# Performance work log

Measured on AMD Instinct MI355X. Metric: run time of the kernel, lower is better.

## Reference

```python
import jax, jax.numpy as jnp
import numpy as np
import math

NUM_HEADS = 16


def setup_inputs() -> dict:
    key = jax.random.key(0)
    ks = jax.random.split(key, 7)
    B, S, D = 2, 2048, 1024
    scale = 1.0 / math.sqrt(D)
    return {
        "query": jax.random.normal(ks[0], (B, S, D), jnp.float32),
        "key": jax.random.normal(ks[1], (B, S, D), jnp.float32),
        "value": jax.random.normal(ks[2], (B, S, D), jnp.float32),
        "Wq": jax.random.normal(ks[3], (D, D), jnp.float32) * scale,
        "Wk": jax.random.normal(ks[4], (D, D), jnp.float32) * scale,
        "Wv": jax.random.normal(ks[5], (D, D), jnp.float32) * scale,
        "Wo": jax.random.normal(ks[6], (D, D), jnp.float32) * scale,
    }


def reference(query, key, value, Wq, Wk, Wv, Wo):
    B, Sq, D = query.shape
    Sk = key.shape[1]
    H = NUM_HEADS
    dk = D // H
    # torch Linear (no bias): y = x @ W.T
    q = (query @ Wq.T).reshape(B, Sq, H, dk).transpose(0, 2, 1, 3)  # [B,H,Sq,dk]
    k = (key @ Wk.T).reshape(B, Sk, H, dk).transpose(0, 2, 1, 3)
    v = (value @ Wv.T).reshape(B, Sk, H, dk).transpose(0, 2, 1, 3)
    scores = jnp.einsum("bhqd,bhkd->bhqk", q, k) / jnp.sqrt(jnp.float32(dk))
    causal = jnp.tril(jnp.ones((Sq, Sk), dtype=bool))  # mask_future=True
    scores = jnp.where(causal[None, None], scores, jnp.float32(-1e9))
    p = jax.nn.softmax(scores, axis=-1)
    x = jnp.einsum("bhqk,bhkd->bhqd", p, v)  # [B,H,Sq,dk]
    x = x.transpose(0, 2, 1, 3).reshape(B, Sq, D)
    return x @ Wo.T
```

## Files before the change

### kernel.cpp

```cpp
#include <hip/hip_runtime.h>
#include <hip/hip_bf16.h>
#include <stdint.h>

#define D_MODEL 1024
#define NHEADS  16
#define DK      64
#define SEQ     2048
#define BATCH   2

typedef __bf16 bf16x8 __attribute__((ext_vector_type(8)));
typedef __bf16 bf16x4 __attribute__((ext_vector_type(4)));
typedef float  f32x4  __attribute__((ext_vector_type(4)));

__device__ __forceinline__ void async_copy16(const void* g, void* l) {
  __builtin_amdgcn_global_load_lds(
      (__attribute__((address_space(1))) void*)g,
      (__attribute__((address_space(3))) void*)l, 16, 0, 0);
}

__global__ void cast3(const float* __restrict__ a, const float* __restrict__ b,
                      const float* __restrict__ c, __bf16* __restrict__ oa,
                      __bf16* __restrict__ ob, __bf16* __restrict__ oc, int n) {
  const float* in = blockIdx.z == 0 ? a : blockIdx.z == 1 ? b : c;
  __bf16* out     = blockIdx.z == 0 ? oa : blockIdx.z == 1 ? ob : oc;
  int i = (blockIdx.x * blockDim.x + threadIdx.x) * 4;
  if (i < n) {
    float4 v = *(const float4*)(in + i);
    bf16x4 o;
    o.x = (__bf16)v.x; o.y = (__bf16)v.y; o.z = (__bf16)v.z; o.w = (__bf16)v.w;
    *(bf16x4*)(out + i) = o;
  }
}

__global__ void cast4(const float* __restrict__ a, const float* __restrict__ b,
                      const float* __restrict__ c, const float* __restrict__ d,
                      __bf16* __restrict__ oa, __bf16* __restrict__ ob,
                      __bf16* __restrict__ oc, __bf16* __restrict__ od, int n) {
  const float* in = blockIdx.z == 0 ? a : blockIdx.z == 1 ? b : blockIdx.z == 2 ? c : d;
  __bf16* out     = blockIdx.z == 0 ? oa : blockIdx.z == 1 ? ob : blockIdx.z == 2 ? oc : od;
  int i = (blockIdx.x * blockDim.x + threadIdx.x) * 4;
  if (i < n) {
    float4 v = *(const float4*)(in + i);
    bf16x4 o;
    o.x = (__bf16)v.x; o.y = (__bf16)v.y; o.z = (__bf16)v.z; o.w = (__bf16)v.w;
    *(bf16x4*)(out + i) = o;
  }
}

template <int BM, int BN, typename OutT>
__global__ __launch_bounds__(256, 2)
void gemm_bt(const __bf16* __restrict__ A0, const __bf16* __restrict__ A1, const __bf16* __restrict__ A2,
             const __bf16* __restrict__ B0, const __bf16* __restrict__ B1, const __bf16* __restrict__ B2,
             OutT* __restrict__ C0, OutT* __restrict__ C1, OutT* __restrict__ C2,
             int M, int N, int K) {
  constexpr int MI = BM / 32, NJ = BN / 32;
  const __bf16* A; const __bf16* Bm; OutT* C;
  if (blockIdx.z == 0)      { A = A0; Bm = B0; C = C0; }
  else if (blockIdx.z == 1) { A = A1; Bm = B1; C = C1; }
  else                      { A = A2; Bm = B2; C = C2; }

  __shared__ __bf16 Ash[BM * 32];
  __shared__ __bf16 Bsh[BN * 32];

  const int tid  = threadIdx.x;
  const int lane = tid & 63;
  const int w    = tid >> 6;
  const int quad = lane >> 4;
  const int l16  = lane & 15;
  const int wr   = w >> 1, wc = w & 1;
  const size_t m0 = (size_t)blockIdx.y * BM;
  const size_t n0 = (size_t)blockIdx.x * BN;

  f32x4 acc[MI][NJ] = {};

  for (int k0 = 0; k0 < K; k0 += 32) {
#pragma unroll
    for (int it = 0; it < BM / 64; ++it) {
      int slot = tid + it * 256;
      async_copy16(A + (m0 + (slot >> 2)) * K + k0 + (slot & 3) * 8, &Ash[slot * 8]);
    }
#pragma unroll
    for (int it = 0; it < BN / 64; ++it) {
      int slot = tid + it * 256;
      async_copy16(Bm + (n0 + (slot >> 2)) * K + k0 + (slot & 3) * 8, &Bsh[slot * 8]);
    }
    __syncthreads();
    bf16x8 af[MI], bfr[NJ];
#pragma unroll
    for (int i = 0; i < MI; ++i)
      af[i] = *(const bf16x8*)&Ash[(wr * (BM / 2) + i * 16 + l16) * 32 + quad * 8];
#pragma unroll
    for (int j = 0; j < NJ; ++j)
      bfr[j] = *(const bf16x8*)&Bsh[(wc * (BN / 2) + j * 16 + l16) * 32 + quad * 8];
#pragma unroll
    for (int i = 0; i < MI; ++i)
#pragma unroll
      for (int j = 0; j < NJ; ++j)
        acc[i][j] = __builtin_amdgcn_mfma_f32_16x16x32_bf16(af[i], bfr[j], acc[i][j], 0, 0, 0);
    __syncthreads();
  }

#pragma unroll
  for (int i = 0; i < MI; ++i)
#pragma unroll
    for (int j = 0; j < NJ; ++j)
#pragma unroll
      for (int r = 0; r < 4; ++r) {
        size_t row = m0 + wr * (BM / 2) + i * 16 + quad * 4 + r;
        size_t col = n0 + wc * (BN / 2) + j * 16 + l16;
        C[row * N + col] = (OutT)acc[i][j][r];
      }
}

__global__ __launch_bounds__(256, 4)
void transpose_v(const __bf16* __restrict__ Vp, __bf16* __restrict__ Vt) {
  __shared__ __bf16 L[64 * 64];
  const int t  = threadIdx.x;
  const int s0 = blockIdx.x * 64, d0 = blockIdx.y * 64, b = blockIdx.z;
#pragma unroll
  for (int it = 0; it < 2; ++it) {
    int slot = t + it * 256;
    int sl = slot >> 3, c = slot & 7;
    int4 v = *(const int4*)&Vp[((size_t)(b * SEQ + s0 + sl)) * D_MODEL + d0 + c * 8];
    *(int4*)&L[sl * 64 + ((c ^ (sl >> 3)) << 3)] = v;
  }
  __syncthreads();
#pragma unroll
  for (int it = 0; it < 2; ++it) {
    int slot = t + it * 256;
    int dl = slot >> 3, c2 = slot & 7;
    __bf16 tmp[8];
#pragma unroll
    for (int e = 0; e < 8; ++e) {
      int rr = c2 * 8 + e;
      tmp[e] = L[rr * 64 + (((dl >> 3) ^ c2) << 3) + (dl & 7)];
    }
    *(int4*)&Vt[((size_t)(b * D_MODEL + d0 + dl)) * SEQ + s0 + c2 * 8] = *(int4*)tmp;
  }
}

#define PS_STRIDE 72

__global__ __launch_bounds__(256, 2)
void attn_kernel(const __bf16* __restrict__ Qp, const __bf16* __restrict__ Kp,
                 const __bf16* __restrict__ Vt, __bf16* __restrict__ Xo) {
  __shared__ __bf16 Kbuf[2][2][64 * 32];
  __shared__ __bf16 Vbuf[2][2][64 * 32];
  __shared__ __bf16 Ps[64 * PS_STRIDE];

  const int tid  = threadIdx.x;
  const int lane = tid & 63;
  const int w    = tid >> 6;
  const int quad = lane >> 4;
  const int l16  = lane & 15;
  const int bh   = blockIdx.x;
  const int pair = blockIdx.y;
  const int b    = bh >> 4, h = bh & 15;
  const size_t baseRow = (size_t)b * SEQ;
  const int colBase = h * DK;

  const int srow = w * 16 + (lane >> 2);
  const int sk   = (lane & 3) * 8;

  const float c1 = 0.18033688011f;
  const float c2 = -23.083120654f;

#pragma unroll 1
  for (int half = 0; half < 2; ++half) {
    const int qt = half == 0 ? (31 - pair) : pair;
    const int q0 = qt * 64;

    bf16x8 aq0, aq1;
    {
      const __bf16* qrow = Qp + (baseRow + q0 + w * 16 + l16) * D_MODEL + colBase;
      aq0 = *(const bf16x8*)(qrow + quad * 8);
      aq1 = *(const bf16x8*)(qrow + 32 + quad * 8);
    }

    f32x4 oacc[4] = {};
    float plsum[4] = {0.f, 0.f, 0.f, 0.f};

    __syncthreads();
    {
      const __bf16* kbase = Kp + (baseRow + srow) * D_MODEL + colBase + sk;
      async_copy16(kbase,      &Kbuf[0][0][srow * 32 + sk]);
      async_copy16(kbase + 32, &Kbuf[0][1][srow * 32 + sk]);
      const __bf16* vbase = Vt + ((size_t)b * D_MODEL + colBase + srow) * SEQ + sk;
      async_copy16(vbase,      &Vbuf[0][0][srow * 32 + sk]);
      async_copy16(vbase + 32, &Vbuf[0][1][srow * 32 + sk]);
    }

    for (int j = 0; j <= qt; ++j) {
      const int bf = j & 1;
      __syncthreads();

      if (j < qt) {
        const int nb = bf ^ 1;
        const __bf16* kbase = Kp + (baseRow + (size_t)(j + 1) * 64 + srow) * D_MODEL + colBase + sk;
        async_copy16(kbase,      &Kbuf[nb][0][srow * 32 + sk]);
        async_copy16(kbase + 32, &Kbuf[nb][1][srow * 32 + sk]);
        const __bf16* vbase = Vt + ((size_t)b * D_MODEL + colBase + srow) * SEQ + (size_t)(j + 1) * 64 + sk;
        async_copy16(vbase,      &Vbuf[nb][0][srow * 32 + sk]);
        async_copy16(vbase + 32, &Vbuf[nb][1][srow * 32 + sk]);
      }

      f32x4 sacc[4] = {};
#pragma unroll
      for (int nt = 0; nt < 4; ++nt) {
        bf16x8 bk = *(const bf16x8*)&Kbuf[bf][0][(nt * 16 + l16) * 32 + quad * 8];
        sacc[nt] = __builtin_amdgcn_mfma_f32_16x16x32_bf16(aq0, bk, sacc[nt], 0, 0, 0);
      }
#pragma unroll
      for (int nt = 0; nt < 4; ++nt) {
        bf16x8 bk = *(const bf16x8*)&Kbuf[bf][1][(nt * 16 + l16) * 32 + quad * 8];
        sacc[nt] = __builtin_amdgcn_mfma_f32_16x16x32_bf16(aq1, bk, sacc[nt], 0, 0, 0);
      }

      const bool diag = (j == qt);
      const int rowg = q0 + w * 16 + quad * 4;
      const int colg = j * 64 + l16;
#pragma unroll
      for (int nt = 0; nt < 4; ++nt)
#pragma unroll
        for (int r = 0; r < 4; ++r) {
          float arg = fmaf(sacc[nt][r], c1, c2);
          if (diag && (colg + nt * 16 > rowg + r)) arg = -1e30f;
          float p = __builtin_amdgcn_exp2f(arg);
          plsum[r] += p;
          Ps[(w * 16 + quad * 4 + r) * PS_STRIDE + nt * 16 + l16] = (__bf16)p;
        }

#pragma unroll
      for (int kc = 0; kc < 2; ++kc) {
        bf16x8 ap = *(const bf16x8*)&Ps[(w * 16 + l16) * PS_STRIDE + kc * 32 + quad * 8];
#pragma unroll
        for (int no = 0; no < 4; ++no) {
          bf16x8 bv = *(const bf16x8*)&Vbuf[bf][kc][(no * 16 + l16) * 32 + quad * 8];
          oacc[no] = __builtin_amdgcn_mfma_f32_16x16x32_bf16(ap, bv, oacc[no], 0, 0, 0);
        }
      }
    }

#pragma unroll
    for (int r = 0; r < 4; ++r) {
      float l = plsum[r];
      for (int off = 1; off < 16; off <<= 1) l += __shfl_xor(l, off, 64);
      float inv = 1.0f / l;
#pragma unroll
      for (int no = 0; no < 4; ++no) {
        size_t row = baseRow + q0 + w * 16 + quad * 4 + r;
        Xo[row * D_MODEL + colBase + no * 16 + l16] = (__bf16)(oacc[no][r] * inv);
      }
    }
  }
}

extern "C" void kernel_launch(void* const* d_in, const int* in_sizes, int n_in,
                              void* d_out, int out_size, void* d_ws, size_t ws_size,
                              hipStream_t stream) {
  const float* q  = (const float*)d_in[0];
  const float* k  = (const float*)d_in[1];
  const float* v  = (const float*)d_in[2];
  const float* wq = (const float*)d_in[3];
  const float* wk = (const float*)d_in[4];
  const float* wv = (const float*)d_in[5];
  const float* wo = (const float*)d_in[6];
  float* out = (float*)d_out;

  const size_t MD = (size_t)BATCH * SEQ * D_MODEL;
  const size_t WD = (size_t)D_MODEL * D_MODEL;
  __bf16* ws  = (__bf16*)d_ws;
  __bf16* Qp  = ws;
  __bf16* Kp  = Qp + MD;
  __bf16* Vp  = Kp + MD;
  __bf16* Xa  = Vp + MD;
  __bf16* qbf = Xa + MD;
  __bf16* kbf = qbf + MD;
  __bf16* vbf = kbf + MD;
  __bf16* wqb = vbf + MD;
  __bf16* wkb = wqb + WD;
  __bf16* wvb = wkb + WD;
  __bf16* wob = wvb + WD;
  __bf16* Vt  = qbf;

  cast3<<<dim3((int)(MD / 1024), 1, 3), 256, 0, stream>>>(q, k, v, qbf, kbf, vbf, (int)MD);
  cast4<<<dim3((int)(WD / 1024), 1, 4), 256, 0, stream>>>(wq, wk, wv, wo, wqb, wkb, wvb, wob, (int)WD);

  gemm_bt<128, 128, __bf16><<<dim3(8, 32, 3), 256, 0, stream>>>(
      qbf, kbf, vbf, wqb, wkb, wvb, Qp, Kp, Vp,
      BATCH * SEQ, D_MODEL, D_MODEL);

  transpose_v<<<dim3(SEQ / 64, D_MODEL / 64, BATCH), 256, 0, stream>>>(Vp, Vt);

  attn_kernel<<<dim3(BATCH * NHEADS, 16), 256, 0, stream>>>(Qp, Kp, Vt, Xa);

  gemm_bt<64, 128, float><<<dim3(8, 64, 1), 256, 0, stream>>>(
      Xa, Xa, Xa, wob, wob, wob, out, out, out,
      BATCH * SEQ, D_MODEL, D_MODEL);
}
```

Measured before the change: 215.3 us.

## Split attention warps across key halves, merge casts, swap GEMM grid order

The attention kernel now gives each of the four warps a 32-row query slab and one half of each 64-key block. Partial outputs and row sums are combined through shared memory at the end, and occupancy is raised to 3 blocks per CU. The two cast kernels are merged into one launch. The GEMM grid mapping is swapped so consecutive blocks walk along M and reuse the same weight tile. The V transpose switches from an XOR swizzle to a padded shared-memory layout with scalar stores. The extra reduction step and the scalar LDS writes in the transpose add cost, and the higher occupancy target may squeeze registers.

Measured after the change: 323.8 us. +50.3%, slower.

```diff
diff --git a/kernel.cpp b/kernel.cpp
--- a/kernel.cpp
+++ b/kernel.cpp
@@ -18,33 +18,32 @@
       (__attribute__((address_space(3))) void*)l, 16, 0, 0);
 }
 
-__global__ void cast3(const float* __restrict__ a, const float* __restrict__ b,
-                      const float* __restrict__ c, __bf16* __restrict__ oa,
-                      __bf16* __restrict__ ob, __bf16* __restrict__ oc, int n) {
-  const float* in = blockIdx.z == 0 ? a : blockIdx.z == 1 ? b : c;
-  __bf16* out     = blockIdx.z == 0 ? oa : blockIdx.z == 1 ? ob : oc;
-  int i = (blockIdx.x * blockDim.x + threadIdx.x) * 4;
-  if (i < n) {
-    float4 v = *(const float4*)(in + i);
-    bf16x4 o;
-    o.x = (__bf16)v.x; o.y = (__bf16)v.y; o.z = (__bf16)v.z; o.w = (__bf16)v.w;
-    *(bf16x4*)(out + i) = o;
-  }
-}
-
-__global__ void cast4(const float* __restrict__ a, const float* __restrict__ b,
-                      const float* __restrict__ c, const float* __restrict__ d,
-                      __bf16* __restrict__ oa, __bf16* __restrict__ ob,
-                      __bf16* __restrict__ oc, __bf16* __restrict__ od, int n) {
-  const float* in = blockIdx.z == 0 ? a : blockIdx.z == 1 ? b : blockIdx.z == 2 ? c : d;
-  __bf16* out     = blockIdx.z == 0 ? oa : blockIdx.z == 1 ? ob : blockIdx.z == 2 ? oc : od;
-  int i = (blockIdx.x * blockDim.x + threadIdx.x) * 4;
-  if (i < n) {
-    float4 v = *(const float4*)(in + i);
-    bf16x4 o;
-    o.x = (__bf16)v.x; o.y = (__bf16)v.y; o.z = (__bf16)v.z; o.w = (__bf16)v.w;
-    *(bf16x4*)(out + i) = o;
-  }
+__global__ void cast_all(const float* __restrict__ q, const float* __restrict__ k,
+                         const float* __restrict__ v, const float* __restrict__ wq,
+                         const float* __restrict__ wk, const float* __restrict__ wv,
+                         const float* __restrict__ wo,
+                         __bf16* __restrict__ oq, __bf16* __restrict__ ok,
+                         __bf16* __restrict__ ov, __bf16* __restrict__ owq,
+                         __bf16* __restrict__ owk, __bf16* __restrict__ owv,
+                         __bf16* __restrict__ owo) {
+  constexpr unsigned Q4 = (unsigned)(BATCH * SEQ * D_MODEL) / 4;
+  constexpr unsigned W4 = (unsigned)(D_MODEL * D_MODEL) / 4;
+  unsigned i = blockIdx.x * 256u + threadIdx.x;
+  const float* in; __bf16* out; unsigned off;
+  if (i < 3 * Q4) {
+    unsigned z = i >> 20; off = i & (Q4 - 1);
+    in  = z == 0 ? q : z == 1 ? k : v;
+    out = z == 0 ? oq : z == 1 ? ok : ov;
+  } else {
+    unsigned j = i - 3 * Q4;
+    unsigned z = j >> 18; off = j & (W4 - 1);
+    in  = z == 0 ? wq : z == 1 ? wk : z == 2 ? wv : wo;
+    out = z == 0 ? owq : z == 1 ? owk : z == 2 ? owv : owo;
+  }
+  float4 val = *(const float4*)(in + (size_t)off * 4);
+  bf16x4 o;
+  o.x = (__bf16)val.x; o.y = (__bf16)val.y; o.z = (__bf16)val.z; o.w = (__bf16)val.w;
+  *(bf16x4*)(out + (size_t)off * 4) = o;
 }
 
 template <int BM, int BN, typename OutT>
@@ -68,8 +67,8 @@
   const int quad = lane >> 4;
   const int l16  = lane & 15;
   const int wr   = w >> 1, wc = w & 1;
-  const size_t m0 = (size_t)blockIdx.y * BM;
-  const size_t n0 = (size_t)blockIdx.x * BN;
+  const size_t m0 = (size_t)blockIdx.x * BM;
+  const size_t n0 = (size_t)blockIdx.y * BN;
 
   f32x4 acc[MI][NJ] = {};
 
@@ -114,7 +113,7 @@
 
 __global__ __launch_bounds__(256, 4)
 void transpose_v(const __bf16* __restrict__ Vp, __bf16* __restrict__ Vt) {
-  __shared__ __bf16 L[64 * 64];
+  __shared__ __bf16 L[64 * 65];
   const int t  = threadIdx.x;
   const int s0 = blockIdx.x * 64, d0 = blockIdx.y * 64, b = blockIdx.z;
 #pragma unroll
@@ -122,7 +121,10 @@
     int slot = t + it * 256;
     int sl = slot >> 3, c = slot & 7;
     int4 v = *(const int4*)&Vp[((size_t)(b * SEQ + s0 + sl)) * D_MODEL + d0 + c * 8];
-    *(int4*)&L[sl * 64 + ((c ^ (sl >> 3)) << 3)] = v;
+    __bf16 tmp[8];
+    *(int4*)tmp = v;
+#pragma unroll
+    for (int e = 0; e < 8; ++e) L[(c * 8 + e) * 65 + sl] = tmp[e];
   }
   __syncthreads();
 #pragma unroll
@@ -131,26 +133,26 @@
     int dl = slot >> 3, c2 = slot & 7;
     __bf16 tmp[8];
 #pragma unroll
-    for (int e = 0; e < 8; ++e) {
-      int rr = c2 * 8 + e;
-      tmp[e] = L[rr * 64 + (((dl >> 3) ^ c2) << 3) + (dl & 7)];
-    }
+    for (int e = 0; e < 8; ++e) tmp[e] = L[dl * 65 + c2 * 8 + e];
     *(int4*)&Vt[((size_t)(b * D_MODEL + d0 + dl)) * SEQ + s0 + c2 * 8] = *(int4*)tmp;
   }
 }
 
-#define PS_STRIDE 72
-
-__global__ __launch_bounds__(256, 2)
+#define PS_W 40
+
+__global__ __launch_bounds__(256, 3)
 void attn_kernel(const __bf16* __restrict__ Qp, const __bf16* __restrict__ Kp,
                  const __bf16* __restrict__ Vt, __bf16* __restrict__ Xo) {
-  __shared__ __bf16 Kbuf[2][2][64 * 32];
-  __shared__ __bf16 Vbuf[2][2][64 * 32];
-  __shared__ __bf16 Ps[64 * PS_STRIDE];
+  __shared__ __bf16 Kb[2 * 2 * 64 * 32];
+  __shared__ __bf16 Vb[2 * 2 * 64 * 32];
+  __shared__ __bf16 Ps[4 * 32 * PS_W];
+  __shared__ float  Xch[2 * 16 * 66];
+  __shared__ float  Lsum[2 * 32];
 
   const int tid  = threadIdx.x;
   const int lane = tid & 63;
   const int w    = tid >> 6;
+  const int qh   = w >> 1, kh = w & 1;
   const int quad = lane >> 4;
   const int l16  = lane & 15;
   const int bh   = blockIdx.x;
@@ -170,24 +172,27 @@
     const int qt = half == 0 ? (31 - pair) : pair;
     const int q0 = qt * 64;
 
-    bf16x8 aq0, aq1;
+    bf16x8 aq[2][2];
     {
-      const __bf16* qrow = Qp + (baseRow + q0 + w * 16 + l16) * D_MODEL + colBase;
-      aq0 = *(const bf16x8*)(qrow + quad * 8);
-      aq1 = *(const bf16x8*)(qrow + 32 + quad * 8);
-    }
-
-    f32x4 oacc[4] = {};
-    float plsum[4] = {0.f, 0.f, 0.f, 0.f};
+      const __bf16* qrow = Qp + (baseRow + q0 + qh * 32 + l16) * D_MODEL + colBase;
+#pragma unroll
+      for (int mt = 0; mt < 2; ++mt)
+#pragma unroll
+        for (int kd = 0; kd < 2; ++kd)
+          aq[mt][kd] = *(const bf16x8*)(qrow + (size_t)mt * 16 * D_MODEL + kd * 32 + quad * 8);
+    }
+
+    f32x4 oacc[2][4] = {};
+    float plsum[2][4] = {};
 
     __syncthreads();
     {
       const __bf16* kbase = Kp + (baseRow + srow) * D_MODEL + colBase + sk;
-      async_copy16(kbase,      &Kbuf[0][0][srow * 32 + sk]);
-      async_copy16(kbase + 32, &Kbuf[0][1][srow * 32 + sk]);
+      async_copy16(kbase,      &Kb[0 * 2048 + srow * 32 + sk]);
+      async_copy16(kbase + 32, &Kb[1 * 2048 + srow * 32 + sk]);
       const __bf16* vbase = Vt + ((size_t)b * D_MODEL + colBase + srow) * SEQ + sk;
-      async_copy16(vbase,      &Vbuf[0][0][srow * 32 + sk]);
-      async_copy16(vbase + 32, &Vbuf[0][1][srow * 32 + sk]);
+      async_copy16(vbase,      &Vb[0 * 2048 + srow * 32 + sk]);
+      async_copy16(vbase + 32, &Vb[1 * 2048 + srow * 32 + sk]);
     }
 
     for (int j = 0; j <= qt; ++j) {
@@ -197,59 +202,91 @@
       if (j < qt) {
         const int nb = bf ^ 1;
         const __bf16* kbase = Kp + (baseRow + (size_t)(j + 1) * 64 + srow) * D_MODEL + colBase + sk;
-        async_copy16(kbase,      &Kbuf[nb][0][srow * 32 + sk]);
-        async_copy16(kbase + 32, &Kbuf[nb][1][srow * 32 + sk]);
+        async_copy16(kbase,      &Kb[(nb * 2 + 0) * 2048 + srow * 32 + sk]);
+        async_copy16(kbase + 32, &Kb[(nb * 2 + 1) * 2048 + srow * 32 + sk]);
         const __bf16* vbase = Vt + ((size_t)b * D_MODEL + colBase + srow) * SEQ + (size_t)(j + 1) * 64 + sk;
-        async_copy16(vbase,      &Vbuf[nb][0][srow * 32 + sk]);
-        async_copy16(vbase + 32, &Vbuf[nb][1][srow * 32 + sk]);
-      }
-
-      f32x4 sacc[4] = {};
-#pragma unroll
-      for (int nt = 0; nt < 4; ++nt) {
-        bf16x8 bk = *(const bf16x8*)&Kbuf[bf][0][(nt * 16 + l16) * 32 + quad * 8];
-        sacc[nt] = __builtin_amdgcn_mfma_f32_16x16x32_bf16(aq0, bk, sacc[nt], 0, 0, 0);
-      }
-#pragma unroll
-      for (int nt = 0; nt < 4; ++nt) {
-        bf16x8 bk = *(const bf16x8*)&Kbuf[bf][1][(nt * 16 + l16) * 32 + quad * 8];
-        sacc[nt] = __builtin_amdgcn_mfma_f32_16x16x32_bf16(aq1, bk, sacc[nt], 0, 0, 0);
+        async_copy16(vbase,      &Vb[(nb * 2 + 0) * 2048 + srow * 32 + sk]);
+        async_copy16(vbase + 32, &Vb[(nb * 2 + 1) * 2048 + srow * 32 + sk]);
+      }
+
+      f32x4 sacc[2][2] = {};
+#pragma unroll
+      for (int kd = 0; kd < 2; ++kd) {
+        bf16x8 bk0 = *(const bf16x8*)&Kb[(bf * 2 + kd) * 2048 + (kh * 32 + l16) * 32 + quad * 8];
+        bf16x8 bk1 = *(const bf16x8*)&Kb[(bf * 2 + kd) * 2048 + (kh * 32 + 16 + l16) * 32 + quad * 8];
+        sacc[0][0] = __builtin_amdgcn_mfma_f32_16x16x32_bf16(aq[0][kd], bk0, sacc[0][0], 0, 0, 0);
+        sacc[0][1] = __builtin_amdgcn_mfma_f32_16x16x32_bf16(aq[0][kd], bk1, sacc[0][1], 0, 0, 0);
+        sacc[1][0] = __builtin_amdgcn_mfma_f32_16x16x32_bf16(aq[1][kd], bk0, sacc[1][0], 0, 0, 0);
+        sacc[1][1] = __builtin_amdgcn_mfma_f32_16x16x32_bf16(aq[1][kd], bk1, sacc[1][1], 0, 0, 0);
       }
 
       const bool diag = (j == qt);
-      const int rowg = q0 + w * 16 + quad * 4;
-      const int colg = j * 64 + l16;
+#pragma unroll
+      for (int mt = 0; mt < 2; ++mt)
+#pragma unroll
+        for (int nt2 = 0; nt2 < 2; ++nt2)
+#pragma unroll
+          for (int r = 0; r < 4; ++r) {
+            float arg = fmaf(sacc[mt][nt2][r], c1, c2);
+            if (diag) {
+              int rowg = q0 + qh * 32 + mt * 16 + quad * 4 + r;
+              int colg = j * 64 + kh * 32 + nt2 * 16 + l16;
+              if (colg > rowg) arg = -1e30f;
+            }
+            float p = __builtin_amdgcn_exp2f(arg);
+            plsum[mt][r] += p;
+            Ps[(w * 32 + mt * 16 + quad * 4 + r) * PS_W + nt2 * 16 + l16] = (__bf16)p;
+          }
+
+      bf16x8 bv[4];
 #pragma unroll
       for (int nt = 0; nt < 4; ++nt)
+        bv[nt] = *(const bf16x8*)&Vb[(bf * 2 + kh) * 2048 + (nt * 16 + l16) * 32 + quad * 8];
+#pragma unroll
+      for (int mt = 0; mt < 2; ++mt) {
+        bf16x8 ap = *(const bf16x8*)&Ps[(w * 32 + mt * 16 + l16) * PS_W + quad * 8];
+#pragma unroll
+        for (int nt = 0; nt < 4; ++nt)
+          oacc[mt][nt] = __builtin_amdgcn_mfma_f32_16x16x32_bf16(ap, bv[nt], oacc[mt][nt], 0, 0, 0);
+      }
+    }
+
+    float lred[2][4];
+#pragma unroll
+    for (int mt = 0; mt < 2; ++mt)
+#pragma unroll
+      for (int r = 0; r < 4; ++r) {
+        float l = plsum[mt][r];
+        for (int off = 1; off < 16; off <<= 1) l += __shfl_xor(l, off, 64);
+        lred[mt][r] = l;
+      }
+
+#pragma unroll 1
+    for (int mt = 0; mt < 2; ++mt) {
+      __syncthreads();
+      if (kh == 1) {
+#pragma unroll
+        for (int nt = 0; nt < 4; ++nt)
+#pragma unroll
+          for (int r = 0; r < 4; ++r)
+            Xch[(qh * 16 + quad * 4 + r) * 66 + nt * 16 + l16] = oacc[mt][nt][r];
+#pragma unroll
+        for (int r = 0; r < 4; ++r)
+          Lsum[qh * 32 + mt * 16 + quad * 4 + r] = lred[mt][r];
+      }
+      __syncthreads();
+      if (kh == 0) {
 #pragma unroll
         for (int r = 0; r < 4; ++r) {
-          float arg = fmaf(sacc[nt][r], c1, c2);
-          if (diag && (colg + nt * 16 > rowg + r)) arg = -1e30f;
-          float p = __builtin_amdgcn_exp2f(arg);
-          plsum[r] += p;
-          Ps[(w * 16 + quad * 4 + r) * PS_STRIDE + nt * 16 + l16] = (__bf16)p;
+          float lt  = lred[mt][r] + Lsum[qh * 32 + mt * 16 + quad * 4 + r];
+          float inv = 1.0f / lt;
+          size_t row = baseRow + q0 + qh * 32 + mt * 16 + quad * 4 + r;
+#pragma unroll
+          for (int nt = 0; nt < 4; ++nt) {
+            float o = oacc[mt][nt][r] + Xch[(qh * 16 + quad * 4 + r) * 66 + nt * 16 + l16];
+            Xo[row * D_MODEL + colBase + nt * 16 + l16] = (__bf16)(o * inv);
+          }
         }
-
-#pragma unroll
-      for (int kc = 0; kc < 2; ++kc) {
-        bf16x8 ap = *(const bf16x8*)&Ps[(w * 16 + l16) * PS_STRIDE + kc * 32 + quad * 8];
-#pragma unroll
-        for (int no = 0; no < 4; ++no) {
-          bf16x8 bv = *(const bf16x8*)&Vbuf[bf][kc][(no * 16 + l16) * 32 + quad * 8];
-          oacc[no] = __builtin_amdgcn_mfma_f32_16x16x32_bf16(ap, bv, oacc[no], 0, 0, 0);
-        }
-      }
-    }
-
-#pragma unroll
-    for (int r = 0; r < 4; ++r) {
-      float l = plsum[r];
-      for (int off = 1; off < 16; off <<= 1) l += __shfl_xor(l, off, 64);
-      float inv = 1.0f / l;
-#pragma unroll
-      for (int no = 0; no < 4; ++no) {
-        size_t row = baseRow + q0 + w * 16 + quad * 4 + r;
-        Xo[row * D_MODEL + colBase + no * 16 + l16] = (__bf16)(oacc[no][r] * inv);
       }
     }
   }
@@ -283,10 +320,10 @@
   __bf16* wob = wvb + WD;
   __bf16* Vt  = qbf;
 
-  cast3<<<dim3((int)(MD / 1024), 1, 3), 256, 0, stream>>>(q, k, v, qbf, kbf, vbf, (int)MD);
-  cast4<<<dim3((int)(WD / 1024), 1, 4), 256, 0, stream>>>(wq, wk, wv, wo, wqb, wkb, wvb, wob, (int)WD);
-
-  gemm_bt<128, 128, __bf16><<<dim3(8, 32, 3), 256, 0, stream>>>(
+  cast_all<<<16384, 256, 0, stream>>>(q, k, v, wq, wk, wv, wo,
+                                      qbf, kbf, vbf, wqb, wkb, wvb, wob);
+
+  gemm_bt<128, 128, __bf16><<<dim3(32, 8, 3), 256, 0, stream>>>(
       qbf, kbf, vbf, wqb, wkb, wvb, Qp, Kp, Vp,
       BATCH * SEQ, D_MODEL, D_MODEL);
 
@@ -294,7 +331,7 @@
 
   attn_kernel<<<dim3(BATCH * NHEADS, 16), 256, 0, stream>>>(Qp, Kp, Vt, Xa);
 
-  gemm_bt<64, 128, float><<<dim3(8, 64, 1), 256, 0, stream>>>(
+  gemm_bt<64, 128, float><<<dim3(64, 8, 1), 256, 0, stream>>>(
       Xa, Xa, Xa, wob, wob, wob, out, out, out,
       BATCH * SEQ, D_MODEL, D_MODEL);
 }
```
